# Kernel optimization log

Measured on AMD Instinct MI355X. Metric: run time of the kernel, lower is better.

Reference implementation:

```python
import jax, jax.numpy as jnp
import numpy as np

B = 65536
H = 256
MINK = jnp.diag(jnp.array([-1.0, 1.0, 1.0, 1.0], dtype=jnp.float32))


def _tetrad(xs, W1, b1, W2, b2):
    # xs: [4] -> e: [4,4]; identity offset keeps e invertible
    h = jnp.tanh(W1 @ xs + b1)
    return jnp.eye(4, dtype=xs.dtype) + 0.1 * (W2 @ h + b2).reshape(4, 4)


def _curv_w(e, de):
    # e: [4,4] tetrad, de: [m,i,j] = d e[i,j] / d x[m]
    e_inv0 = jnp.linalg.inv(e).T            # torch permute [0,2,1]
    e_inv = e_inv0 @ MINK                   # 'mj,ji->mi'
    pw = jnp.einsum('ni,mnj->mij', e_inv, de)
    pr = jnp.einsum('mij,mk->kij', pw, e_inv)
    tau = pr - pr.transpose(1, 0, 2)        # torch permute [0,2,1,3]
    r = (tau + tau.transpose(2, 1, 0) + tau.transpose(2, 0, 1)) / 2
    r = jnp.einsum('ljk,li->ijk', r, MINK)
    return jnp.einsum('ijk,mi->mjk', r, e)  # w: [m,j,k]


def _per_sample(xs, W1, b1, W2, b2):
    tet = lambda z: _tetrad(z, W1, b1, W2, b2)

    def w_of_x(z):
        e = tet(z)
        de = jnp.moveaxis(jax.jacfwd(tet)(z), -1, 0)  # [m,i,j]
        return _curv_w(e, de)

    w = w_of_x(xs)                                    # [4,4,4]
    dw = jnp.moveaxis(jax.jacfwd(w_of_x)(xs), -1, 0)  # [m,i,j,k]
    e = tet(xs)
    e_inv0 = jnp.linalg.inv(e).T
    return w, dw, e, e_inv0, e_inv0 @ MINK


def setup_inputs() -> dict:
    key = jax.random.key(0)
    ks = jax.random.split(key, 5)
    x = jax.random.normal(ks[0], (B, 4), dtype=jnp.float32)
    W1 = jax.random.normal(ks[1], (H, 4), dtype=jnp.float32) * 0.5
    b1 = jax.random.normal(ks[2], (H,), dtype=jnp.float32) * 0.1
    W2 = jax.random.normal(ks[3], (16, H), dtype=jnp.float32) * (0.5 / np.sqrt(H))
    b2 = jax.random.normal(ks[4], (16,), dtype=jnp.float32) * 0.1
    return {"x": x, "W1": W1, "b1": b1, "W2": W2, "b2": b2}


def reference(x, W1, b1, W2, b2):
    w, dw, e, e_inv0, e_inv = jax.vmap(
        _per_sample, in_axes=(0, None, None, None, None)
    )(x, W1, b1, W2, b2)
    w2 = jnp.einsum('bmik,kj->bmij', w, MINK)
    # NOTE: the two scalar einsums below faithfully reproduce the original
    # torch code ('bmik,bnkj->' reduces to a scalar); they cancel analytically.
    riemann = (dw - dw.transpose(0, 2, 1, 3, 4)
               + jnp.einsum('bmik,bnkj->', w2, w)
               - jnp.einsum('bnik,bmkj->', w2, w))
    ricci = jnp.einsum('bmnij,bnj->bmi', riemann, e_inv0)
    ricci = jnp.einsum('bmj,bmi->bij', ricci, e_inv)
    riemann = jnp.einsum('bmnij,bmk->bknij', riemann, e_inv)
    riemann = jnp.einsum('bknij,bnl->bklij', riemann, e_inv)
    return ricci, riemann
```

## Files before the change

kernel.cpp:

```cpp
#include <hip/hip_runtime.h>
#include <cstdint>
#include <cstddef>


typedef _Float16 h2   __attribute__((ext_vector_type(2)));
typedef _Float16 f16x8 __attribute__((ext_vector_type(8)));
typedef float    f32x4 __attribute__((ext_vector_type(4)));

#define WAVES 4
#define ITERS 8

__device__ __forceinline__ void wfence() {
  asm volatile("s_waitcnt lgkmcnt(0)" ::: "memory");
  __builtin_amdgcn_sched_barrier(0);
}

__device__ __forceinline__ unsigned pkrtz(float a, float b) {
#if __has_builtin(__builtin_amdgcn_cvt_pkrtz)
  return __builtin_bit_cast(unsigned, __builtin_amdgcn_cvt_pkrtz(a, b));
#else
  h2 v; v[0] = (_Float16)a; v[1] = (_Float16)b;
  return __builtin_bit_cast(unsigned, v);
#endif
}

__global__ __launch_bounds__(256, 3) void ein_kernel(
    const float* __restrict__ x, const float* __restrict__ W1,
    const float* __restrict__ b1, const float* __restrict__ W2,
    const float* __restrict__ b2, float* __restrict__ out, int B)
{
  __shared__ __align__(16) _Float16 Gt[WAVES][16][264];
  __shared__ __align__(16) float Qs[WAVES][320];
  __shared__ __align__(16) float dde2[WAVES][320];
  __shared__ __align__(16) float A_s[WAVES][16];
  __shared__ float F_s[WAVES][64];
  __shared__ float U_s[WAVES][64];
  __shared__ float Ad_s[WAVES][64];
  __shared__ __align__(16) float R_s[WAVES][96];
  __shared__ float rp_s[WAVES][16];

  const int tid  = threadIdx.x;
  const int wv   = tid >> 6;
  const int lane = tid & 63;
  const int l15  = lane & 15;
  const int hb   = lane >> 4;
  const int dd = lane >> 4, ii = (lane >> 2) & 3, jj = lane & 3;
  const float eta_ii = (ii == 0) ? -1.f : 1.f;

  const float4 w1A = ((const float4*)W1)[2*lane];
  const float4 w1B = ((const float4*)W1)[2*lane + 1];
  const float4 w1C = ((const float4*)W1)[2*lane + 128];
  const float4 w1D = ((const float4*)W1)[2*lane + 129];
  const float b1A = b1[2*lane],       b1B = b1[2*lane + 1];
  const float b1C = b1[2*lane + 128], b1D = b1[2*lane + 129];
  f16x8 afr[8];
  #pragma unroll
  for (int cc = 0; cc < 8; ++cc) {
    const float* p = W2 + l15*256 + cc*32 + hb*8;
    float4 u0 = ((const float4*)p)[0];
    float4 u1 = ((const float4*)p)[1];
    f16x8 a;
    a[0]=(_Float16)u0.x; a[1]=(_Float16)u0.y; a[2]=(_Float16)u0.z; a[3]=(_Float16)u0.w;
    a[4]=(_Float16)u1.x; a[5]=(_Float16)u1.y; a[6]=(_Float16)u1.z; a[7]=(_Float16)u1.w;
    afr[cc] = a;
  }
  const float eb0 = b2[4*hb+0], eb1 = b2[4*hb+1], eb2 = b2[4*hb+2], eb3 = b2[4*hb+3];

  float* out0 = out;
  float* out1 = out + (size_t)B * 16;

  auto neuron = [](const float4& w, float b, const float4& xs,
                   float& h, float4& gw4, float4& uw4) {
    float z = b + w.x*xs.x + w.y*xs.y + w.z*xs.z + w.w*xs.w;
    float t  = __expf(-2.f * fabsf(z));
    float r1 = __builtin_amdgcn_rcpf(1.f + t);
    float habs = (1.f - t) * r1;
    h = (z < 0.f) ? -habs : habs;
    float g = 4.f * t * r1 * r1;
    float u = -2.f * h * g;
    gw4 = make_float4(g*w.x, g*w.y, g*w.z, g*w.w);
    uw4 = make_float4(u*w.x, u*w.y, u*w.z, u*w.w);
  };

  const int sbase = blockIdx.x * (WAVES * ITERS);
  float4 xs = ((const float4*)x)[sbase + wv];

  for (int it = 0; it < ITERS; ++it) {
    const int s = sbase + it * WAVES + wv;
    const float4 xc = xs;
    if (it + 1 < ITERS) xs = ((const float4*)x)[sbase + (it + 1) * WAVES + wv];

    unsigned* gwp = (unsigned*)&Gt[wv][0][2*lane];
    {
      float hA, hB; float4 gA, gB, uA, uB;
      neuron(w1A, b1A, xc, hA, gA, uA);
      neuron(w1B, b1B, xc, hB, gB, uB);
      gwp[0*132] = pkrtz(hA, hB);
      gwp[1*132] = pkrtz(gA.x, gB.x);  gwp[2*132] = pkrtz(gA.y, gB.y);
      gwp[3*132] = pkrtz(gA.z, gB.z);  gwp[4*132] = pkrtz(gA.w, gB.w);
      gwp[5*132]  = pkrtz(uA.x*w1A.x, uB.x*w1B.x);
      gwp[6*132]  = pkrtz(uA.x*w1A.y, uB.x*w1B.y);
      gwp[7*132]  = pkrtz(uA.x*w1A.z, uB.x*w1B.z);
      gwp[8*132]  = pkrtz(uA.x*w1A.w, uB.x*w1B.w);
      gwp[9*132]  = pkrtz(uA.y*w1A.y, uB.y*w1B.y);
      gwp[10*132] = pkrtz(uA.y*w1A.z, uB.y*w1B.z);
      gwp[11*132] = pkrtz(uA.y*w1A.w, uB.y*w1B.w);
      gwp[12*132] = pkrtz(uA.z*w1A.z, uB.z*w1B.z);
      gwp[13*132] = pkrtz(uA.z*w1A.w, uB.z*w1B.w);
      gwp[14*132] = pkrtz(uA.w*w1A.w, uB.w*w1B.w);
    }
    {
      float hA, hB; float4 gA, gB, uA, uB;
      neuron(w1C, b1C, xc, hA, gA, uA);
      neuron(w1D, b1D, xc, hB, gB, uB);
      gwp[0*132+64] = pkrtz(hA, hB);
      gwp[1*132+64] = pkrtz(gA.x, gB.x);  gwp[2*132+64] = pkrtz(gA.y, gB.y);
      gwp[3*132+64] = pkrtz(gA.z, gB.z);  gwp[4*132+64] = pkrtz(gA.w, gB.w);
      gwp[5*132+64]  = pkrtz(uA.x*w1C.x, uB.x*w1D.x);
      gwp[6*132+64]  = pkrtz(uA.x*w1C.y, uB.x*w1D.y);
      gwp[7*132+64]  = pkrtz(uA.x*w1C.z, uB.x*w1D.z);
      gwp[8*132+64]  = pkrtz(uA.x*w1C.w, uB.x*w1D.w);
      gwp[9*132+64]  = pkrtz(uA.y*w1C.y, uB.y*w1D.y);
      gwp[10*132+64] = pkrtz(uA.y*w1C.z, uB.y*w1D.z);
      gwp[11*132+64] = pkrtz(uA.y*w1C.w, uB.y*w1D.w);
      gwp[12*132+64] = pkrtz(uA.z*w1C.z, uB.z*w1D.z);
      gwp[13*132+64] = pkrtz(uA.z*w1C.w, uB.z*w1D.w);
      gwp[14*132+64] = pkrtz(uA.w*w1C.w, uB.w*w1D.w);
    }
    wfence();

    f32x4 acc = {0.f, 0.f, 0.f, 0.f};
    {
      const f16x8* gp = (const f16x8*)&Gt[wv][l15][hb*8];
      #pragma unroll
      for (int cc = 0; cc < 8; ++cc) {
        f16x8 bfr = gp[cc * 4];
        acc = __builtin_amdgcn_mfma_f32_16x16x32_f16(afr[cc], bfr, acc, 0, 0, 0);
      }
    }
    {
      float v0 = 0.1f*acc[0], v1 = 0.1f*acc[1], v2 = 0.1f*acc[2], v3 = 0.1f*acc[3];
      if (l15 == 0) {
        v0 += 0.1f*eb0 + ((hb == 0) ? 1.f : 0.f);
        v1 += 0.1f*eb1 + ((hb == 1) ? 1.f : 0.f);
        v2 += 0.1f*eb2 + ((hb == 2) ? 1.f : 0.f);
        v3 += 0.1f*eb3 + ((hb == 3) ? 1.f : 0.f);
      }
      float4 v4 = make_float4(v0, v1, v2, v3);
      *(float4*)&Qs[wv][l15*20 + hb*4] = v4;
      if (l15 >= 5 && l15 <= 14) {
        int t = l15 - 5;
        int p = (t >= 9) ? 3 : (t >= 7) ? 2 : (t >= 4) ? 1 : 0;
        int q = t - ((p * (7 - p)) >> 1);
        *(float4*)&dde2[wv][(p*4 + q)*20 + hb*4] = v4;
        if (p != q) *(float4*)&dde2[wv][(q*4 + p)*20 + hb*4] = v4;
      }
    }
    wfence();

    {
      float4 er0 = *(const float4*)&Qs[wv][0];
      float4 er1 = *(const float4*)&Qs[wv][4];
      float4 er2 = *(const float4*)&Qs[wv][8];
      float4 er3 = *(const float4*)&Qs[wv][12];
      float m00=er0.x,m01=er0.y,m02=er0.z,m03=er0.w;
      float m10=er1.x,m11=er1.y,m12=er1.z,m13=er1.w;
      float m20=er2.x,m21=er2.y,m22=er2.z,m23=er2.w;
      float m30=er3.x,m31=er3.y,m32=er3.z,m33=er3.w;
      float s0_=m00*m11-m01*m10, s1_=m00*m12-m02*m10, s2_=m00*m13-m03*m10;
      float s3_=m01*m12-m02*m11, s4_=m01*m13-m03*m11, s5_=m02*m13-m03*m12;
      float c5_=m22*m33-m23*m32, c4_=m21*m33-m23*m31, c3_=m21*m32-m22*m31;
      float c2_=m20*m33-m23*m30, c1_=m20*m32-m22*m30, c0_=m20*m31-m21*m30;
      float det = s0_*c5_ - s1_*c4_ + s2_*c3_ + s3_*c2_ - s4_*c1_ + s5_*c0_;
      float inv = 1.0f / det;
      if (lane == 0) {
        *(float4*)&A_s[wv][0]  = make_float4(( m11*c5_-m12*c4_+m13*c3_)*inv,
                                             (-m01*c5_+m02*c4_-m03*c3_)*inv,
                                             ( m31*s5_-m32*s4_+m33*s3_)*inv,
                                             (-m21*s5_+m22*s4_-m23*s3_)*inv);
        *(float4*)&A_s[wv][4]  = make_float4((-m10*c5_+m12*c2_-m13*c1_)*inv,
                                             ( m00*c5_-m02*c2_+m03*c1_)*inv,
                                             (-m30*s5_+m32*s2_-m33*s1_)*inv,
                                             ( m20*s5_-m22*s2_+m23*s1_)*inv);
        *(float4*)&A_s[wv][8]  = make_float4(( m10*c4_-m11*c2_+m13*c0_)*inv,
                                             (-m00*c4_+m01*c2_-m03*c0_)*inv,
                                             ( m30*s4_-m31*s2_+m33*s0_)*inv,
                                             (-m20*s4_+m21*s2_-m23*s0_)*inv);
        *(float4*)&A_s[wv][12] = make_float4((-m10*c3_+m11*c1_-m12*c0_)*inv,
                                             ( m00*c3_-m01*c1_+m02*c0_)*inv,
                                             (-m30*s3_+m31*s1_-m32*s0_)*inv,
                                             ( m20*s3_-m21*s1_+m22*s0_)*inv);
      }
    }
    wfence();

    F_s[wv][dd*16 + ii*4 + jj] = Qs[wv][(1+dd)*20 + ii*4 + jj]
                               - Qs[wv][(1+ii)*20 + dd*4 + jj];
    {
      float4 Ai = *(const float4*)&A_s[wv][ii*4];
      U_s[wv][dd*16 + ii*4 + jj] =
          Ai.x * Qs[wv][(1+dd)*20 +  0 + jj] + Ai.y * Qs[wv][(1+dd)*20 +  4 + jj]
        + Ai.z * Qs[wv][(1+dd)*20 +  8 + jj] + Ai.w * Qs[wv][(1+dd)*20 + 12 + jj];
    }
    wfence();

    {
      float4 Ur = *(const float4*)&U_s[wv][dd*16 + ii*4];
      Ad_s[wv][dd*16 + ii*4 + jj] =
        -(Ur.x * A_s[wv][0 + jj] + Ur.y * A_s[wv][4 + jj]
        + Ur.z * A_s[wv][8 + jj] + Ur.w * A_s[wv][12 + jj]);
    }
    wfence();

    {
      auto riem = [&](int m, int n) -> float {
        float4 Adm = *(const float4*)&Ad_s[wv][m*16 + ii*4];
        float4 Adn = *(const float4*)&Ad_s[wv][n*16 + ii*4];
        float4 Aiv = *(const float4*)&A_s[wv][ii*4];
        float a;
        a  = Adm.x * F_s[wv][n*16 +  0 + jj] - Adn.x * F_s[wv][m*16 +  0 + jj]
           + Aiv.x * (dde2[wv][(n*4+0)*20 + m*4 + jj] - dde2[wv][(m*4+0)*20 + n*4 + jj]);
        a += Adm.y * F_s[wv][n*16 +  4 + jj] - Adn.y * F_s[wv][m*16 +  4 + jj]
           + Aiv.y * (dde2[wv][(n*4+1)*20 + m*4 + jj] - dde2[wv][(m*4+1)*20 + n*4 + jj]);
        a += Adm.z * F_s[wv][n*16 +  8 + jj] - Adn.z * F_s[wv][m*16 +  8 + jj]
           + Aiv.z * (dde2[wv][(n*4+2)*20 + m*4 + jj] - dde2[wv][(m*4+2)*20 + n*4 + jj]);
        a += Adm.w * F_s[wv][n*16 + 12 + jj] - Adn.w * F_s[wv][m*16 + 12 + jj]
           + Aiv.w * (dde2[wv][(n*4+3)*20 + m*4 + jj] - dde2[wv][(m*4+3)*20 + n*4 + jj]);
        return 0.5f * eta_ii * a;
      };
      int m1 = (dd < 3) ? 0 : 1;
      int n1 = (dd < 3) ? (dd + 1) : 2;
      R_s[wv][dd*16 + ii*4 + jj] = riem(m1, n1);
      if (dd < 2)
        R_s[wv][(4 + dd)*16 + ii*4 + jj] = riem(dd + 1, 3);
    }
    wfence();

    {
      const int kl = lane >> 2, kk = kl >> 2, ll = kl & 3, i2 = lane & 3;
      float4 akv = *(const float4*)&A_s[wv][kk*4];
      float4 alv = *(const float4*)&A_s[wv][ll*4];
      float sgn = ((kk == 0) != (ll == 0)) ? -1.f : 1.f;
      float B0 = (akv.x*alv.y - akv.y*alv.x) * sgn;
      float B1 = (akv.x*alv.z - akv.z*alv.x) * sgn;
      float B2 = (akv.x*alv.w - akv.w*alv.x) * sgn;
      float B3 = (akv.y*alv.z - akv.z*alv.y) * sgn;
      float B4 = (akv.y*alv.w - akv.w*alv.y) * sgn;
      float B5 = (akv.z*alv.w - akv.w*alv.z) * sgn;
      float4 r0 = *(const float4*)&R_s[wv][ 0 + i2*4];
      float4 r1 = *(const float4*)&R_s[wv][16 + i2*4];
      float4 r2 = *(const float4*)&R_s[wv][32 + i2*4];
      float4 r3 = *(const float4*)&R_s[wv][48 + i2*4];
      float4 r4 = *(const float4*)&R_s[wv][64 + i2*4];
      float4 r5 = *(const float4*)&R_s[wv][80 + i2*4];
      float4 o;
      o.x = B0*r0.x + B1*r1.x + B2*r2.x + B3*r3.x + B4*r4.x + B5*r5.x;
      o.y = B0*r0.y + B1*r1.y + B2*r2.y + B3*r3.y + B4*r4.y + B5*r5.y;
      o.z = B0*r0.z + B1*r1.z + B2*r2.z + B3*r3.z + B4*r4.z + B5*r5.z;
      o.w = B0*r0.w + B1*r1.w + B2*r2.w + B3*r3.w + B4*r4.w + B5*r5.w;
      ((float4*)(out1 + ((size_t)s << 8)))[kl*4 + i2] = o;
    }
    if (ii == 0) {
      const int m = dd, ip = jj;
      float a = 0.f;
      #pragma unroll
      for (int n = 0; n < 4; ++n) {
        if (n != m) {
          int mm = (m < n) ? m : n;
          int nn = (m < n) ? n : m;
          int pr = mm * (7 - mm) / 2 + (nn - mm - 1);
          float sg = (m < n) ? 1.f : -1.f;
          float4 rr = *(const float4*)&R_s[wv][pr*16 + ip*4];
          a += sg * (rr.x * A_s[wv][0 + n] + rr.y * A_s[wv][4 + n]
                   + rr.z * A_s[wv][8 + n] + rr.w * A_s[wv][12 + n]);
        }
      }
      rp_s[wv][m*4 + ip] = a;
    }
    wfence();
    if (dd == 0) {
      float4 Ai = *(const float4*)&A_s[wv][ii*4];
      float a = Ai.x * rp_s[wv][0 + jj] + Ai.y * rp_s[wv][4 + jj]
              + Ai.z * rp_s[wv][8 + jj] + Ai.w * rp_s[wv][12 + jj];
      out0[(size_t)s * 16 + ii*4 + jj] = eta_ii * a;
    }
  }
}

extern "C" void kernel_launch(void* const* d_in, const int* in_sizes, int n_in,
                              void* d_out, int out_size, void* d_ws, size_t ws_size,
                              hipStream_t stream) {
  (void)n_in; (void)out_size; (void)d_ws; (void)ws_size;
  const float* x  = (const float*)d_in[0];
  const float* W1 = (const float*)d_in[1];
  const float* b1 = (const float*)d_in[2];
  const float* W2 = (const float*)d_in[3];
  const float* b2 = (const float*)d_in[4];
  float* out = (float*)d_out;
  const int B = in_sizes[0] / 4;
  const int nblk = B / (WAVES * ITERS);
  hipLaunchKernelGGL(ein_kernel, dim3(nblk), dim3(256), 0, stream,
                     x, W1, b1, W2, b2, out, B);
}
```

Measured before the change: 171.1 us.

## Halve Gt staging buffer, split MFMA into two halves, shuffle instead of LDS

The per-wave fp16 staging tile Gt is halved to 128 neurons, and the 256-neuron contraction now runs as two stage-then-MFMA passes over the same buffer. This cuts LDS per block, and launch bounds rise from 3 to 5 blocks per CU to raise occupancy. ITERS drops from 8 to 4, giving more, shorter blocks. The U_s LDS round trip and one fence are replaced by 4-wide lane shuffles. In exchange, the split adds extra fences and serialises staging with the MFMAs, and the tighter launch bound may force register spills.

```diff
diff --git a/kernel.cpp b/kernel.cpp
--- a/kernel.cpp
+++ b/kernel.cpp
@@ -8,7 +8,7 @@
 typedef float    f32x4 __attribute__((ext_vector_type(4)));
 
 #define WAVES 4
-#define ITERS 8
+#define ITERS 4
 
 __device__ __forceinline__ void wfence() {
   asm volatile("s_waitcnt lgkmcnt(0)" ::: "memory");
@@ -24,17 +24,16 @@
 #endif
 }
 
-__global__ __launch_bounds__(256, 3) void ein_kernel(
+__global__ __launch_bounds__(256, 5) void ein_kernel(
     const float* __restrict__ x, const float* __restrict__ W1,
     const float* __restrict__ b1, const float* __restrict__ W2,
     const float* __restrict__ b2, float* __restrict__ out, int B)
 {
-  __shared__ __align__(16) _Float16 Gt[WAVES][16][264];
+  __shared__ __align__(16) _Float16 Gt[WAVES][16][136];
   __shared__ __align__(16) float Qs[WAVES][320];
   __shared__ __align__(16) float dde2[WAVES][320];
   __shared__ __align__(16) float A_s[WAVES][16];
   __shared__ float F_s[WAVES][64];
-  __shared__ float U_s[WAVES][64];
   __shared__ float Ad_s[WAVES][64];
   __shared__ __align__(16) float R_s[WAVES][96];
   __shared__ float rp_s[WAVES][16];
@@ -90,54 +89,44 @@
     const float4 xc = xs;
     if (it + 1 < ITERS) xs = ((const float4*)x)[sbase + (it + 1) * WAVES + wv];
 
-    unsigned* gwp = (unsigned*)&Gt[wv][0][2*lane];
-    {
+    unsigned* gwp = (unsigned*)&Gt[wv][0][0] + lane;
+    auto stage_pair = [&](const float4& wA, float bA_, const float4& wB, float bB_) {
       float hA, hB; float4 gA, gB, uA, uB;
-      neuron(w1A, b1A, xc, hA, gA, uA);
-      neuron(w1B, b1B, xc, hB, gB, uB);
-      gwp[0*132] = pkrtz(hA, hB);
-      gwp[1*132] = pkrtz(gA.x, gB.x);  gwp[2*132] = pkrtz(gA.y, gB.y);
-      gwp[3*132] = pkrtz(gA.z, gB.z);  gwp[4*132] = pkrtz(gA.w, gB.w);
-      gwp[5*132]  = pkrtz(uA.x*w1A.x, uB.x*w1B.x);
-      gwp[6*132]  = pkrtz(uA.x*w1A.y, uB.x*w1B.y);
-      gwp[7*132]  = pkrtz(uA.x*w1A.z, uB.x*w1B.z);
-      gwp[8*132]  = pkrtz(uA.x*w1A.w, uB.x*w1B.w);
-      gwp[9*132]  = pkrtz(uA.y*w1A.y, uB.y*w1B.y);
-      gwp[10*132] = pkrtz(uA.y*w1A.z, uB.y*w1B.z);
-      gwp[11*132] = pkrtz(uA.y*w1A.w, uB.y*w1B.w);
-      gwp[12*132] = pkrtz(uA.z*w1A.z, uB.z*w1B.z);
-      gwp[13*132] = pkrtz(uA.z*w1A.w, uB.z*w1B.w);
-      gwp[14*132] = pkrtz(uA.w*w1A.w, uB.w*w1B.w);
-    }
-    {
-      float hA, hB; float4 gA, gB, uA, uB;
-      neuron(w1C, b1C, xc, hA, gA, uA);
-      neuron(w1D, b1D, xc, hB, gB, uB);
-      gwp[0*132+64] = pkrtz(hA, hB);
-      gwp[1*132+64] = pkrtz(gA.x, gB.x);  gwp[2*132+64] = pkrtz(gA.y, gB.y);
-      gwp[3*132+64] = pkrtz(gA.z, gB.z);  gwp[4*132+64] = pkrtz(gA.w, gB.w);
-      gwp[5*132+64]  = pkrtz(uA.x*w1C.x, uB.x*w1D.x);
-      gwp[6*132+64]  = pkrtz(uA.x*w1C.y, uB.x*w1D.y);
-      gwp[7*132+64]  = pkrtz(uA.x*w1C.z, uB.x*w1D.z);
-      gwp[8*132+64]  = pkrtz(uA.x*w1C.w, uB.x*w1D.w);
-      gwp[9*132+64]  = pkrtz(uA.y*w1C.y, uB.y*w1D.y);
-      gwp[10*132+64] = pkrtz(uA.y*w1C.z, uB.y*w1D.z);
-      gwp[11*132+64] = pkrtz(uA.y*w1C.w, uB.y*w1D.w);
-      gwp[12*132+64] = pkrtz(uA.z*w1C.z, uB.z*w1D.z);
-      gwp[13*132+64] = pkrtz(uA.z*w1C.w, uB.z*w1D.w);
-      gwp[14*132+64] = pkrtz(uA.w*w1C.w, uB.w*w1D.w);
-    }
-    wfence();
+      neuron(wA, bA_, xc, hA, gA, uA);
+      neuron(wB, bB_, xc, hB, gB, uB);
+      gwp[0*68] = pkrtz(hA, hB);
+      gwp[1*68] = pkrtz(gA.x, gB.x);  gwp[2*68] = pkrtz(gA.y, gB.y);
+      gwp[3*68] = pkrtz(gA.z, gB.z);  gwp[4*68] = pkrtz(gA.w, gB.w);
+      gwp[5*68]  = pkrtz(uA.x*wA.x, uB.x*wB.x);
+      gwp[6*68]  = pkrtz(uA.x*wA.y, uB.x*wB.y);
+      gwp[7*68]  = pkrtz(uA.x*wA.z, uB.x*wB.z);
+      gwp[8*68]  = pkrtz(uA.x*wA.w, uB.x*wB.w);
+      gwp[9*68]  = pkrtz(uA.y*wA.y, uB.y*wB.y);
+      gwp[10*68] = pkrtz(uA.y*wA.z, uB.y*wB.z);
+      gwp[11*68] = pkrtz(uA.y*wA.w, uB.y*wB.w);
+      gwp[12*68] = pkrtz(uA.z*wA.z, uB.z*wB.z);
+      gwp[13*68] = pkrtz(uA.z*wA.w, uB.z*wB.w);
+      gwp[14*68] = pkrtz(uA.w*wA.w, uB.w*wB.w);
+    };
+    const f16x8* gp = (const f16x8*)&Gt[wv][l15][hb*8];
 
     f32x4 acc = {0.f, 0.f, 0.f, 0.f};
-    {
-      const f16x8* gp = (const f16x8*)&Gt[wv][l15][hb*8];
-      #pragma unroll
-      for (int cc = 0; cc < 8; ++cc) {
-        f16x8 bfr = gp[cc * 4];
-        acc = __builtin_amdgcn_mfma_f32_16x16x32_f16(afr[cc], bfr, acc, 0, 0, 0);
-      }
-    }
+    stage_pair(w1A, b1A, w1B, b1B);
+    wfence();
+    #pragma unroll
+    for (int kk = 0; kk < 4; ++kk) {
+      f16x8 bfr = gp[kk * 4];
+      acc = __builtin_amdgcn_mfma_f32_16x16x32_f16(afr[kk], bfr, acc, 0, 0, 0);
+    }
+    wfence();
+    stage_pair(w1C, b1C, w1D, b1D);
+    wfence();
+    #pragma unroll
+    for (int kk = 0; kk < 4; ++kk) {
+      f16x8 bfr = gp[kk * 4];
+      acc = __builtin_amdgcn_mfma_f32_16x16x32_f16(afr[4 + kk], bfr, acc, 0, 0, 0);
+    }
+
     {
       float v0 = 0.1f*acc[0], v1 = 0.1f*acc[1], v2 = 0.1f*acc[2], v3 = 0.1f*acc[3];
       if (l15 == 0) {
@@ -198,17 +187,14 @@
                                - Qs[wv][(1+ii)*20 + dd*4 + jj];
     {
       float4 Ai = *(const float4*)&A_s[wv][ii*4];
-      U_s[wv][dd*16 + ii*4 + jj] =
+      float u =
           Ai.x * Qs[wv][(1+dd)*20 +  0 + jj] + Ai.y * Qs[wv][(1+dd)*20 +  4 + jj]
         + Ai.z * Qs[wv][(1+dd)*20 +  8 + jj] + Ai.w * Qs[wv][(1+dd)*20 + 12 + jj];
-    }
-    wfence();
-
-    {
-      float4 Ur = *(const float4*)&U_s[wv][dd*16 + ii*4];
-      Ad_s[wv][dd*16 + ii*4 + jj] =
-        -(Ur.x * A_s[wv][0 + jj] + Ur.y * A_s[wv][4 + jj]
-        + Ur.z * A_s[wv][8 + jj] + Ur.w * A_s[wv][12 + jj]);
+      float Adv = -( __shfl(u, 0, 4) * A_s[wv][ 0 + jj]
+                   + __shfl(u, 1, 4) * A_s[wv][ 4 + jj]
+                   + __shfl(u, 2, 4) * A_s[wv][ 8 + jj]
+                   + __shfl(u, 3, 4) * A_s[wv][12 + jj] );
+      Ad_s[wv][dd*16 + ii*4 + jj] = Adv;
     }
     wfence();
 
```

Result: slower. 338.9 us (+98.1%).
